# Kernel tuning notes

Measured on AMD Instinct MI355X. Metric: run time of the kernel, lower is better.

Reference implementation:

```python
import jax, jax.numpy as jnp
import numpy as np

C = 256
SHAPE = (4, 256, 32, 32, 32)  # B, C, D, H, W


def setup_inputs() -> dict:
    key = jax.random.key(0)
    ks = jax.random.split(key, 8)
    scale = 1.0 / np.sqrt(C)
    return {
        "x": jax.random.normal(ks[0], SHAPE, dtype=jnp.float32),
        "y": jax.random.normal(ks[1], SHAPE, dtype=jnp.float32),
        "Wq": jax.random.normal(ks[2], (C, C), dtype=jnp.float32) * scale,
        "bq": jax.random.normal(ks[3], (C,), dtype=jnp.float32) * 0.01,
        "Wk": jax.random.normal(ks[4], (C, C), dtype=jnp.float32) * scale,
        "bk": jax.random.normal(ks[5], (C,), dtype=jnp.float32) * 0.01,
        "Wv": jax.random.normal(ks[6], (C, C), dtype=jnp.float32) * scale,
        "bv": jax.random.normal(ks[7], (C,), dtype=jnp.float32) * 0.01,
    }


def _proj_flat(v, W, b):
    # 1x1x1 Conv3d == per-voxel linear over channels. v: [B,C,D,H,W] -> [B,C,N]
    B, Cc = v.shape[0], v.shape[1]
    vf = v.reshape(B, Cc, -1)  # [B, C, N]
    return jnp.einsum("oc,bcn->bon", W, vf) + b[None, :, None]


def reference(x, y, Wq, bq, Wk, bk, Wv, bv):
    spatial = y.shape[2:]
    q = _proj_flat(x, Wq, bq)  # [B, C, N]
    k = _proj_flat(y, Wk, bk)  # [B, C, N]
    v = _proj_flat(y, Wv, bv)  # [B, C, N]
    # channel-attention: scores[b, i, j] = sum_n q[b,i,n] * k[b,j,n]  (unscaled)
    scores = jnp.einsum("bin,bjn->bij", q, k)  # [B, C, C]
    weights = jax.nn.softmax(scores, axis=2)
    fused = jnp.einsum("bij,bjn->bin", weights, v)  # [B, C, N]
    return fused.reshape(fused.shape[0], fused.shape[1], *spatial)
```

## Files before the change

kernel.cpp:

```cpp
#include <hip/hip_runtime.h>

#define Bb 4
#define Cc 256
#define Nn 32768

typedef short s16x8 __attribute__((ext_vector_type(8)));
typedef float f32x4 __attribute__((ext_vector_type(4)));
typedef float f32x4v __attribute__((ext_vector_type(4)));

__device__ __forceinline__ unsigned short bfh(float f) {
    union { float f; unsigned u; } c; c.f = f;
    unsigned u = c.u + 0x7fffu + ((c.u >> 16) & 1u);
    return (unsigned short)(u >> 16);
}
__device__ __forceinline__ unsigned fbits(float f) {
    union { float f; unsigned u; } c; c.f = f; return c.u;
}
__device__ __forceinline__ float fof(unsigned u) {
    union { unsigned u; float f; } c; c.u = u; return c.f;
}
__device__ __forceinline__ int swz(int l) { return l ^ ((l >> 3) & 6); }

__device__ __forceinline__ void cvt8(f32x4v A, f32x4v B, uint4& h, uint4& l) {
    unsigned a0 = fbits(A.x), a1 = fbits(A.y), a2 = fbits(A.z), a3 = fbits(A.w);
    unsigned b0 = fbits(B.x), b1 = fbits(B.y), b2 = fbits(B.z), b3 = fbits(B.w);
    h.x = __builtin_amdgcn_perm(a1, a0, 0x07060302u);
    h.y = __builtin_amdgcn_perm(a3, a2, 0x07060302u);
    h.z = __builtin_amdgcn_perm(b1, b0, 0x07060302u);
    h.w = __builtin_amdgcn_perm(b3, b2, 0x07060302u);
    unsigned l0 = fbits(A.x - fof(a0 & 0xffff0000u)) + 0x8000u;
    unsigned l1 = fbits(A.y - fof(a1 & 0xffff0000u)) + 0x8000u;
    unsigned l2 = fbits(A.z - fof(a2 & 0xffff0000u)) + 0x8000u;
    unsigned l3 = fbits(A.w - fof(a3 & 0xffff0000u)) + 0x8000u;
    unsigned m0 = fbits(B.x - fof(b0 & 0xffff0000u)) + 0x8000u;
    unsigned m1 = fbits(B.y - fof(b1 & 0xffff0000u)) + 0x8000u;
    unsigned m2 = fbits(B.z - fof(b2 & 0xffff0000u)) + 0x8000u;
    unsigned m3 = fbits(B.w - fof(b3 & 0xffff0000u)) + 0x8000u;
    l.x = __builtin_amdgcn_perm(l1, l0, 0x07060302u);
    l.y = __builtin_amdgcn_perm(l3, l2, 0x07060302u);
    l.z = __builtin_amdgcn_perm(m1, m0, 0x07060302u);
    l.w = __builtin_amdgcn_perm(m3, m2, 0x07060302u);
}
__device__ __forceinline__ float s4(f32x4v v) { return (v.x + v.y) + (v.z + v.w); }

__global__ __launch_bounds__(512, 2) void k_gram(const float* __restrict__ x,
                                                 const float* __restrict__ y,
                                                 float* __restrict__ part,
                                                 float* __restrict__ sxp,
                                                 float* __restrict__ syp,
                                                 int nsplit) {
    extern __shared__ short smem[];

    int G = Bb * nsplit * 2;
    int chunk = G >> 3;
    int lid = blockIdx.x;
    int bid = (lid & 7) * chunk + (lid >> 3);

    int half = bid & 1;
    int ks = (bid >> 1) % nsplit;
    int b = bid / (2 * nsplit);
    int Kblk = Nn / nsplit;
    int nstep = Kblk >> 5;

    const float* X = x + (size_t)b * Cc * Nn + (size_t)(half * 128) * Nn + (size_t)ks * Kblk;
    const float* Y = y + (size_t)b * Cc * Nn + (size_t)ks * Kblk;

    int tid = threadIdx.x;
    int lane = tid & 63;
    int wave = tid >> 6;
    int wr = wave >> 2, wc = wave & 3;

    int xr = tid >> 2, xq = tid & 3;
    const float* px = X + (size_t)xr * Nn + xq * 8;
    int xl = (xr & 15) + 16 * xq;
    int xo = ((xr >> 4) * 64 + swz(xl)) * 8;
    int yr = tid >> 1, yh2 = tid & 1;
    const float* py = Y + (size_t)yr * Nn + yh2 * 16;
    int yl0 = (yr & 15) + 32 * yh2, yl1 = yl0 + 16;
    int yo0 = ((yr >> 4) * 64 + swz(yl0)) * 8;
    int yo1 = ((yr >> 4) * 64 + swz(yl1)) * 8;

    f32x4 acc[4][4];
    #pragma unroll
    for (int i = 0; i < 4; ++i)
        #pragma unroll
        for (int j = 0; j < 4; ++j)
            #pragma unroll
            for (int z = 0; z < 4; ++z) acc[i][j][z] = 0.f;

    float xsum = 0.f, ysum = 0.f;
    f32x4v A0[2], B0[4], A1[2], B1[4];

    #define LDX(A, B, kb) do { \
        A[0] = __builtin_nontemporal_load((const f32x4v*)(px + (kb)) + 0); \
        A[1] = __builtin_nontemporal_load((const f32x4v*)(px + (kb)) + 1); \
        B[0] = ((const f32x4v*)(py + (kb)))[0]; B[1] = ((const f32x4v*)(py + (kb)))[1]; \
        B[2] = ((const f32x4v*)(py + (kb)))[2]; B[3] = ((const f32x4v*)(py + (kb)))[3]; \
    } while (0)

    #define COMPUTE(Sb) do { \
        int sl = swz(lane); \
        s16x8 ah[4], al[4]; \
        _Pragma("unroll") \
        for (int i = 0; i < 4; ++i) { \
            int fr = (wr * 4 + i) * 64 + sl; \
            ah[i] = *(const s16x8*)&(Sb)[fr * 8]; \
            al[i] = *(const s16x8*)&(Sb)[4096 + fr * 8]; \
        } \
        _Pragma("unroll") \
        for (int j = 0; j < 4; ++j) { \
            int fr = (wc * 4 + j) * 64 + sl; \
            s16x8 bh = *(const s16x8*)&(Sb)[8192 + fr * 8]; \
            s16x8 bl = *(const s16x8*)&(Sb)[16384 + fr * 8]; \
            _Pragma("unroll") \
            for (int i = 0; i < 4; ++i) { \
                acc[i][j] = __builtin_amdgcn_mfma_f32_16x16x32_bf16(ah[i], bh, acc[i][j], 0, 0, 0); \
                acc[i][j] = __builtin_amdgcn_mfma_f32_16x16x32_bf16(ah[i], bl, acc[i][j], 0, 0, 0); \
                acc[i][j] = __builtin_amdgcn_mfma_f32_16x16x32_bf16(al[i], bh, acc[i][j], 0, 0, 0); \
            } \
        } \
    } while (0)

    #define GSTEP(A, B, nkb, donext, cur) do { \
        uint4 hx, qxv, hy0, qy0, hy1, qy1; \
        cvt8(A[0], A[1], hx, qxv); \
        cvt8(B[0], B[1], hy0, qy0); \
        cvt8(B[2], B[3], hy1, qy1); \
        xsum += s4(A[0]) + s4(A[1]); \
        if (half == 0) ysum += s4(B[0]) + s4(B[1]) + s4(B[2]) + s4(B[3]); \
        short* Sb = smem + (cur); \
        *(uint4*)&Sb[xo] = hx;  *(uint4*)&Sb[4096 + xo] = qxv; \
        *(uint4*)&Sb[8192 + yo0] = hy0; *(uint4*)&Sb[16384 + yo0] = qy0; \
        *(uint4*)&Sb[8192 + yo1] = hy1; *(uint4*)&Sb[16384 + yo1] = qy1; \
        if (donext) LDX(A, B, nkb); \
        asm volatile("s_waitcnt lgkmcnt(0)" ::: "memory"); \
        __builtin_amdgcn_sched_barrier(0); \
        __builtin_amdgcn_s_barrier(); \
        __builtin_amdgcn_sched_barrier(0); \
        COMPUTE(Sb); \
    } while (0)

    LDX(A0, B0, 0);
    LDX(A1, B1, 32);
    for (int t = 0; t < nstep; t += 2) {
        GSTEP(A0, B0, (t + 2) * 32, t + 2 < nstep, 0);
        GSTEP(A1, B1, (t + 3) * 32, t + 3 < nstep, 24576);
    }
    #undef GSTEP
    #undef COMPUTE
    #undef LDX

    xsum += __shfl_xor(xsum, 1);
    xsum += __shfl_xor(xsum, 2);
    ysum += __shfl_xor(ysum, 1);
    if (xq == 0) sxp[((size_t)b * nsplit + ks) * 256 + half * 128 + xr] = xsum;
    if (half == 0 && yh2 == 0) syp[((size_t)b * nsplit + ks) * 256 + yr] = ysum;

    float* P = part + ((size_t)b * nsplit + ks) * Cc * Cc;
    #pragma unroll
    for (int i = 0; i < 4; ++i)
        #pragma unroll
        for (int j = 0; j < 4; ++j)
            #pragma unroll
            for (int reg = 0; reg < 4; ++reg) {
                int gi = half * 128 + wr * 64 + i * 16 + (lane >> 4) * 4 + reg;
                int gj = wc * 64 + j * 16 + (lane & 15);
                P[(size_t)gi * Cc + gj] = acc[i][j][reg];
            }
}

__global__ __launch_bounds__(256) void k_reduceS(const float* __restrict__ part,
                                                 const float* __restrict__ sxp,
                                                 const float* __restrict__ syp,
                                                 float* __restrict__ S,
                                                 float* __restrict__ sx,
                                                 float* __restrict__ sy, int split) {
    if (blockIdx.x < 256) {
        int t = blockIdx.x * 256 + threadIdx.x;
        int b = t >> 14;
        int rc = t & 16383;
        f32x4v s = {0.f, 0.f, 0.f, 0.f};
        for (int ks = 0; ks < split; ++ks) {
            f32x4v v = ((const f32x4v*)(part + (((size_t)b * split + ks) << 16)))[rc];
            s += v;
        }
        ((f32x4v*)S)[t] = s;
    } else {
        int flat = (blockIdx.x - 256) * 256 + threadIdx.x;
        int b = flat >> 9, rem = flat & 511, which = rem >> 8, c = rem & 255;
        const float* src = (which ? syp : sxp) + (size_t)b * split * 256 + c;
        float s = 0.f;
        for (int ks = 0; ks < split; ++ks) s += src[(size_t)ks * 256];
        (which ? sy : sx)[b * 256 + c] = s;
    }
}

__global__ __launch_bounds__(256) void k_attn(const float* __restrict__ S,
                                              const float* __restrict__ sx,
                                              const float* __restrict__ sy,
                                              const float* __restrict__ Wq,
                                              const float* __restrict__ Wk,
                                              const float* __restrict__ Wv,
                                              const float* __restrict__ bq,
                                              const float* __restrict__ bk,
                                              const float* __restrict__ bv,
                                              short* __restrict__ Mbf,
                                              float* __restrict__ cb) {
    __shared__ float wq_lds[8][256];
    __shared__ float u_lds[8][256];
    __shared__ float p_lds[8][256];
    __shared__ float wv_lds[32][256];
    __shared__ float sx_lds[256], sy_lds[256];
    __shared__ float qx_lds[8];

    int b = blockIdx.x >> 5;
    int i0 = (blockIdx.x & 31) << 3;
    int tid = threadIdx.x;
    int lane = tid & 63, wv4 = tid >> 6;

    float bqv[8];
    #pragma unroll
    for (int ii = 0; ii < 8; ++ii) {
        wq_lds[ii][tid] = Wq[(size_t)(i0 + ii) * Cc + tid];
        bqv[ii] = bq[i0 + ii];
    }
    sx_lds[tid] = sx[b * Cc + tid];
    sy_lds[tid] = sy[b * Cc + tid];
    __syncthreads();

    float u[8] = {};
    const float* Sb = S + (size_t)b * Cc * Cc + tid;
    #pragma unroll 4
    for (int c = 0; c < Cc; ++c) {
        float s = Sb[(size_t)c * Cc];
        #pragma unroll
        for (int ii = 0; ii < 8; ++ii) u[ii] += wq_lds[ii][c] * s;
    }
    #pragma unroll
    for (int ii = 0; ii < 8; ++ii) u_lds[ii][tid] = u[ii] + bqv[ii] * sy_lds[tid];

    #pragma unroll
    for (int rr = 0; rr < 2; ++rr) {
        int ii = wv4 * 2 + rr;
        float p = 0.f;
        #pragma unroll
        for (int k = 0; k < 4; ++k) { int c = lane + 64 * k; p += wq_lds[ii][c] * sx_lds[c]; }
        #pragma unroll
        for (int m = 1; m < 64; m <<= 1) p += __shfl_xor(p, m);
        if (lane == 0) qx_lds[ii] = p;
    }
    __syncthreads();

    float sc[8] = {};
    const float* WkRow = Wk + (size_t)tid * Cc;
    for (int ch = 0; ch < 8; ++ch) {
        float wkr[32];
        #pragma unroll
        for (int k = 0; k < 8; ++k)
            *(float4*)&wkr[4 * k] = ((const float4*)(WkRow + ch * 32))[k];
        #pragma unroll
        for (int dd = 0; dd < 32; ++dd) {
            float w = wkr[dd];
            #pragma unroll
            for (int ii = 0; ii < 8; ++ii) sc[ii] += u_lds[ii][ch * 32 + dd] * w;
        }
    }
    float bkj = bk[tid];
    #pragma unroll
    for (int ii = 0; ii < 8; ++ii) {
        sc[ii] += (qx_lds[ii] + 32768.0f * bqv[ii]) * bkj;
        p_lds[ii][tid] = sc[ii];
    }
    __syncthreads();

    #pragma unroll
    for (int rr = 0; rr < 2; ++rr) {
        int ii = wv4 * 2 + rr;
        float v0 = p_lds[ii][lane], v1 = p_lds[ii][lane + 64];
        float v2 = p_lds[ii][lane + 128], v3 = p_lds[ii][lane + 192];
        float mx = fmaxf(fmaxf(v0, v1), fmaxf(v2, v3));
        #pragma unroll
        for (int m = 1; m < 64; m <<= 1) mx = fmaxf(mx, __shfl_xor(mx, m));
        float e0 = expf(v0 - mx), e1 = expf(v1 - mx), e2 = expf(v2 - mx), e3 = expf(v3 - mx);
        float ssum = (e0 + e1) + (e2 + e3);
        #pragma unroll
        for (int m = 1; m < 64; m <<= 1) ssum += __shfl_xor(ssum, m);
        float inv = 1.0f / ssum;
        float w0 = e0 * inv, w1 = e1 * inv, w2 = e2 * inv, w3 = e3 * inv;
        p_lds[ii][lane] = w0; p_lds[ii][lane + 64] = w1;
        p_lds[ii][lane + 128] = w2; p_lds[ii][lane + 192] = w3;
        float cbp = w0 * bv[lane] + w1 * bv[lane + 64] + w2 * bv[lane + 128] + w3 * bv[lane + 192];
        #pragma unroll
        for (int m = 1; m < 64; m <<= 1) cbp += __shfl_xor(cbp, m);
        if (lane == 0) cb[b * Cc + i0 + ii] = cbp;
    }
    __syncthreads();

    float m[8] = {};
    for (int jc = 0; jc < 8; ++jc) {
        #pragma unroll
        for (int k = 0; k < 8; ++k) {
            int fidx = k * 256 + tid;
            int jj = fidx >> 6, f4 = fidx & 63;
            *(float4*)&wv_lds[jj][4 * f4] =
                *(const float4*)(Wv + (size_t)(jc * 32 + jj) * Cc + 4 * f4);
        }
        __syncthreads();
        #pragma unroll 4
        for (int jj = 0; jj < 32; ++jj) {
            float w = wv_lds[jj][tid];
            #pragma unroll
            for (int ii = 0; ii < 8; ++ii) m[ii] += p_lds[ii][jc * 32 + jj] * w;
        }
        __syncthreads();
    }
    #pragma unroll
    for (int ii = 0; ii < 8; ++ii)
        Mbf[((size_t)(b * Cc + i0 + ii)) * Cc + tid] = (short)bfh(m[ii]);
}

__global__ __launch_bounds__(512, 2) void k_out_mfma(const short* __restrict__ Mbf,
                                                     const float* __restrict__ y,
                                                     const float* __restrict__ cb,
                                                     float* __restrict__ out) {
    int tid = threadIdx.x;
    int lane = tid & 63;
    int wave = tid >> 6;
    int wr = wave >> 2, wc = wave & 3;
    int bid = blockIdx.x;
    int b = bid >> 8, grp = bid & 255;
    int nbase = grp * 128 + wc * 32;
    const float* Y = y + (size_t)b * Cc * Nn;
    const short* M = Mbf + (size_t)b * Cc * Cc;
    int l15 = lane & 15;
    int cbase = 8 * (lane >> 4);
    int n0 = nbase + l15;

    f32x4 acc[8][2];
    #pragma unroll
    for (int ti = 0; ti < 8; ++ti)
        #pragma unroll
        for (int nb = 0; nb < 2; ++nb)
            #pragma unroll
            for (int z = 0; z < 4; ++z) acc[ti][nb][z] = 0.f;

    s16x8 af0[8], af1[8];
    float ya0[8], yb0[8], ya1[8], yb1[8];

    #define AFLD(AF, s) do { int c0 = 32 * (s) + cbase; \
        _Pragma("unroll") \
        for (int ti = 0; ti < 8; ++ti) \
            AF[ti] = *(const s16x8*)&M[(size_t)(wr * 128 + ti * 16 + l15) * Cc + c0]; \
        } while (0)

    #define LDY(YA, YB, s) do { int c0 = 32 * (s) + cbase; \
        _Pragma("unroll") \
        for (int j = 0; j < 8; ++j) { \
            YA[j] = Y[(size_t)(c0 + j) * Nn + n0]; \
            YB[j] = Y[(size_t)(c0 + j) * Nn + n0 + 16]; \
        } } while (0)

    #define OSTEP(AF, AFN, YA, YB, s) do { \
        s16x8 bf0, bf1; \
        _Pragma("unroll") \
        for (int j = 0; j < 8; ++j) { bf0[j] = (short)bfh(YA[j]); bf1[j] = (short)bfh(YB[j]); } \
        if ((s) + 1 < 8) AFLD(AFN, (s) + 1); \
        if ((s) + 2 < 8) LDY(YA, YB, (s) + 2); \
        _Pragma("unroll") \
        for (int ti = 0; ti < 8; ++ti) { \
            acc[ti][0] = __builtin_amdgcn_mfma_f32_16x16x32_bf16(AF[ti], bf0, acc[ti][0], 0, 0, 0); \
            acc[ti][1] = __builtin_amdgcn_mfma_f32_16x16x32_bf16(AF[ti], bf1, acc[ti][1], 0, 0, 0); \
        } } while (0)

    AFLD(af0, 0);
    LDY(ya0, yb0, 0);
    LDY(ya1, yb1, 1);
    for (int s = 0; s < 8; s += 2) {
        OSTEP(af0, af1, ya0, yb0, s);
        OSTEP(af1, af0, ya1, yb1, s + 1);
    }
    #undef OSTEP
    #undef LDY
    #undef AFLD

    #pragma unroll
    for (int ti = 0; ti < 8; ++ti)
        #pragma unroll
        for (int nb = 0; nb < 2; ++nb)
            #pragma unroll
            for (int reg = 0; reg < 4; ++reg) {
                int i = wr * 128 + ti * 16 + (lane >> 4) * 4 + reg;
                out[((size_t)b * Cc + i) * Nn + nbase + nb * 16 + l15] =
                    acc[ti][nb][reg] + cb[b * Cc + i];
            }
}

extern "C" void kernel_launch(void* const* d_in, const int* in_sizes, int n_in,
                              void* d_out, int out_size, void* d_ws, size_t ws_size,
                              hipStream_t stream) {
    const float* x  = (const float*)d_in[0];
    const float* y  = (const float*)d_in[1];
    const float* Wq = (const float*)d_in[2];
    const float* bq = (const float*)d_in[3];
    const float* Wk = (const float*)d_in[4];
    const float* bk = (const float*)d_in[5];
    const float* Wv = (const float*)d_in[6];
    const float* bv = (const float*)d_in[7];
    float* out = (float*)d_out;

    float* ws = (float*)d_ws;
    size_t off = 0;
    float* S  = ws + off; off += (size_t)Bb * Cc * Cc;
    float* sx = ws + off; off += Bb * Cc;
    float* sy = ws + off; off += Bb * Cc;
    short* Mbf = (short*)(ws + off); off += (size_t)Bb * Cc * Cc / 2;
    float* cb = ws + off; off += Bb * Cc;
    float* sxp = ws + off; off += (size_t)Bb * 64 * 256;
    float* syp = ws + off; off += (size_t)Bb * 64 * 256;
    float* part = ws + off;

    size_t avail = ws_size / 4 - off;
    int split = 32;
    while (split > 16 && (size_t)split * Bb * Cc * Cc > avail) split >>= 1;

    (void)hipFuncSetAttribute(reinterpret_cast<const void*>(k_gram),
                              hipFuncAttributeMaxDynamicSharedMemorySize, 98304);

    k_gram<<<Bb * split * 2, 512, 98304, stream>>>(x, y, part, sxp, syp, split);
    k_reduceS<<<264, 256, 0, stream>>>(part, sxp, syp, S, sx, sy, split);
    k_attn<<<Bb * 32, 256, 0, stream>>>(S, sx, sy, Wq, Wk, Wv, bq, bk, bv, Mbf, cb);
    k_out_mfma<<<1024, 512, 0, stream>>>(Mbf, y, cb, out);
}
```

Baseline: 221.1 us.

## Load gram MFMA operands directly from global into registers, dropping LDS staging

The gram kernel no longer stages bf16 hi/lo splits in shared memory behind a barrier. Each lane now loads its MFMA fragments straight from global memory, converts them in registers, and computes a 128x128 quadrant per 256-thread block, with four quadrant blocks per split. This removes LDS traffic and block barriers. In exchange the x and y data are each read twice from global memory across the quadrant blocks, and every lane reads 8 strided rows, which may hurt coalescing and raise register pressure.

```diff
diff --git a/kernel.cpp b/kernel.cpp
--- a/kernel.cpp
+++ b/kernel.cpp
@@ -19,7 +19,6 @@
 __device__ __forceinline__ float fof(unsigned u) {
     union { unsigned u; float f; } c; c.u = u; return c.f;
 }
-__device__ __forceinline__ int swz(int l) { return l ^ ((l >> 3) & 6); }
 
 __device__ __forceinline__ void cvt8(f32x4v A, f32x4v B, uint4& h, uint4& l) {
     unsigned a0 = fbits(A.x), a1 = fbits(A.y), a2 = fbits(A.z), a3 = fbits(A.w);
@@ -43,42 +42,39 @@
 }
 __device__ __forceinline__ float s4(f32x4v v) { return (v.x + v.y) + (v.z + v.w); }
 
-__global__ __launch_bounds__(512, 2) void k_gram(const float* __restrict__ x,
+__global__ __launch_bounds__(256, 2) void k_gram(const float* __restrict__ x,
                                                  const float* __restrict__ y,
                                                  float* __restrict__ part,
                                                  float* __restrict__ sxp,
                                                  float* __restrict__ syp,
                                                  int nsplit) {
-    extern __shared__ short smem[];
-
-    int G = Bb * nsplit * 2;
+    int G = Bb * nsplit * 4;
     int chunk = G >> 3;
     int lid = blockIdx.x;
     int bid = (lid & 7) * chunk + (lid >> 3);
 
-    int half = bid & 1;
-    int ks = (bid >> 1) % nsplit;
-    int b = bid / (2 * nsplit);
+    int quad = bid & 3;
+    int ti = quad >> 1, tj = quad & 1;
+    int ks = (bid >> 2) % nsplit;
+    int b  = bid / (4 * nsplit);
     int Kblk = Nn / nsplit;
     int nstep = Kblk >> 5;
-
-    const float* X = x + (size_t)b * Cc * Nn + (size_t)(half * 128) * Nn + (size_t)ks * Kblk;
-    const float* Y = y + (size_t)b * Cc * Nn + (size_t)ks * Kblk;
 
     int tid = threadIdx.x;
     int lane = tid & 63;
     int wave = tid >> 6;
-    int wr = wave >> 2, wc = wave & 3;
-
-    int xr = tid >> 2, xq = tid & 3;
-    const float* px = X + (size_t)xr * Nn + xq * 8;
-    int xl = (xr & 15) + 16 * xq;
-    int xo = ((xr >> 4) * 64 + swz(xl)) * 8;
-    int yr = tid >> 1, yh2 = tid & 1;
-    const float* py = Y + (size_t)yr * Nn + yh2 * 16;
-    int yl0 = (yr & 15) + 32 * yh2, yl1 = yl0 + 16;
-    int yo0 = ((yr >> 4) * 64 + swz(yl0)) * 8;
-    int yo1 = ((yr >> 4) * 64 + swz(yl1)) * 8;
+    int wwr = wave >> 1, wwc = wave & 1;
+    int l15 = lane & 15, lh = lane >> 4;
+
+    const float* Xb = x + (size_t)b * Cc * Nn + (size_t)ks * Kblk + lh * 8;
+    const float* Yb = y + (size_t)b * Cc * Nn + (size_t)ks * Kblk + lh * 8;
+    const float* ap[4];
+    const float* bp[4];
+    #pragma unroll
+    for (int i = 0; i < 4; ++i) {
+        ap[i] = Xb + (size_t)(ti * 128 + wwr * 64 + i * 16 + l15) * Nn;
+        bp[i] = Yb + (size_t)(tj * 128 + wwc * 64 + i * 16 + l15) * Nn;
+    }
 
     f32x4 acc[4][4];
     #pragma unroll
@@ -88,73 +84,72 @@
             #pragma unroll
             for (int z = 0; z < 4; ++z) acc[i][j][z] = 0.f;
 
-    float xsum = 0.f, ysum = 0.f;
-    f32x4v A0[2], B0[4], A1[2], B1[4];
-
-    #define LDX(A, B, kb) do { \
-        A[0] = __builtin_nontemporal_load((const f32x4v*)(px + (kb)) + 0); \
-        A[1] = __builtin_nontemporal_load((const f32x4v*)(px + (kb)) + 1); \
-        B[0] = ((const f32x4v*)(py + (kb)))[0]; B[1] = ((const f32x4v*)(py + (kb)))[1]; \
-        B[2] = ((const f32x4v*)(py + (kb)))[2]; B[3] = ((const f32x4v*)(py + (kb)))[3]; \
-    } while (0)
-
-    #define COMPUTE(Sb) do { \
-        int sl = swz(lane); \
-        s16x8 ah[4], al[4]; \
+    float xs[4] = {0.f, 0.f, 0.f, 0.f};
+    float ys[4] = {0.f, 0.f, 0.f, 0.f};
+
+    f32x4v A0[8], B0[8], A1[8], B1[8];
+
+    #define GLD(AS, BS, kb) do { \
         _Pragma("unroll") \
         for (int i = 0; i < 4; ++i) { \
-            int fr = (wr * 4 + i) * 64 + sl; \
-            ah[i] = *(const s16x8*)&(Sb)[fr * 8]; \
-            al[i] = *(const s16x8*)&(Sb)[4096 + fr * 8]; \
+            AS[2 * i]     = ((const f32x4v*)(ap[i] + (kb)))[0]; \
+            AS[2 * i + 1] = ((const f32x4v*)(ap[i] + (kb)))[1]; \
+            BS[2 * i]     = ((const f32x4v*)(bp[i] + (kb)))[0]; \
+            BS[2 * i + 1] = ((const f32x4v*)(bp[i] + (kb)))[1]; \
+        } } while (0)
+
+    #define GSTEP(AS, BS, nkb, donext) do { \
+        s16x8 Ah[4], Al[4], Bh[4], Bl[4]; \
+        _Pragma("unroll") \
+        for (int i = 0; i < 4; ++i) { \
+            uint4 h, q; \
+            cvt8(AS[2 * i], AS[2 * i + 1], h, q); \
+            Ah[i] = __builtin_bit_cast(s16x8, h); \
+            Al[i] = __builtin_bit_cast(s16x8, q); \
+            if (wwc == 0) xs[i] += s4(AS[2 * i]) + s4(AS[2 * i + 1]); \
+            cvt8(BS[2 * i], BS[2 * i + 1], h, q); \
+            Bh[i] = __builtin_bit_cast(s16x8, h); \
+            Bl[i] = __builtin_bit_cast(s16x8, q); \
+            if (wwr == 0) ys[i] += s4(BS[2 * i]) + s4(BS[2 * i + 1]); \
         } \
-        _Pragma("unroll") \
-        for (int j = 0; j < 4; ++j) { \
-            int fr = (wc * 4 + j) * 64 + sl; \
-            s16x8 bh = *(const s16x8*)&(Sb)[8192 + fr * 8]; \
-            s16x8 bl = *(const s16x8*)&(Sb)[16384 + fr * 8]; \
+        if (donext) GLD(AS, BS, nkb); \
+        _Pragma("unroll") \
+        for (int j = 0; j < 4; ++j) \
             _Pragma("unroll") \
             for (int i = 0; i < 4; ++i) { \
-                acc[i][j] = __builtin_amdgcn_mfma_f32_16x16x32_bf16(ah[i], bh, acc[i][j], 0, 0, 0); \
-                acc[i][j] = __builtin_amdgcn_mfma_f32_16x16x32_bf16(ah[i], bl, acc[i][j], 0, 0, 0); \
-                acc[i][j] = __builtin_amdgcn_mfma_f32_16x16x32_bf16(al[i], bh, acc[i][j], 0, 0, 0); \
+                acc[i][j] = __builtin_amdgcn_mfma_f32_16x16x32_bf16(Ah[i], Bh[j], acc[i][j], 0, 0, 0); \
+                acc[i][j] = __builtin_amdgcn_mfma_f32_16x16x32_bf16(Ah[i], Bl[j], acc[i][j], 0, 0, 0); \
+                acc[i][j] = __builtin_amdgcn_mfma_f32_16x16x32_bf16(Al[i], Bh[j], acc[i][j], 0, 0, 0); \
             } \
-        } \
-    } while (0)
-
-    #define GSTEP(A, B, nkb, donext, cur) do { \
-        uint4 hx, qxv, hy0, qy0, hy1, qy1; \
-        cvt8(A[0], A[1], hx, qxv); \
-        cvt8(B[0], B[1], hy0, qy0); \
-        cvt8(B[2], B[3], hy1, qy1); \
-        xsum += s4(A[0]) + s4(A[1]); \
-        if (half == 0) ysum += s4(B[0]) + s4(B[1]) + s4(B[2]) + s4(B[3]); \
-        short* Sb = smem + (cur); \
-        *(uint4*)&Sb[xo] = hx;  *(uint4*)&Sb[4096 + xo] = qxv; \
-        *(uint4*)&Sb[8192 + yo0] = hy0; *(uint4*)&Sb[16384 + yo0] = qy0; \
-        *(uint4*)&Sb[8192 + yo1] = hy1; *(uint4*)&Sb[16384 + yo1] = qy1; \
-        if (donext) LDX(A, B, nkb); \
-        asm volatile("s_waitcnt lgkmcnt(0)" ::: "memory"); \
-        __builtin_amdgcn_sched_barrier(0); \
-        __builtin_amdgcn_s_barrier(); \
-        __builtin_amdgcn_sched_barrier(0); \
-        COMPUTE(Sb); \
-    } while (0)
-
-    LDX(A0, B0, 0);
-    LDX(A1, B1, 32);
+        } while (0)
+
+    GLD(A0, B0, 0);
+    GLD(A1, B1, 32);
     for (int t = 0; t < nstep; t += 2) {
-        GSTEP(A0, B0, (t + 2) * 32, t + 2 < nstep, 0);
-        GSTEP(A1, B1, (t + 3) * 32, t + 3 < nstep, 24576);
+        GSTEP(A0, B0, (t + 2) * 32, t + 2 < nstep);
+        GSTEP(A1, B1, (t + 3) * 32, t + 3 < nstep);
     }
     #undef GSTEP
-    #undef COMPUTE
-    #undef LDX
-
-    xsum += __shfl_xor(xsum, 1);
-    xsum += __shfl_xor(xsum, 2);
-    ysum += __shfl_xor(ysum, 1);
-    if (xq == 0) sxp[((size_t)b * nsplit + ks) * 256 + half * 128 + xr] = xsum;
-    if (half == 0 && yh2 == 0) syp[((size_t)b * nsplit + ks) * 256 + yr] = ysum;
+    #undef GLD
+
+    #pragma unroll
+    for (int i = 0; i < 4; ++i) {
+        xs[i] += __shfl_xor(xs[i], 16);
+        xs[i] += __shfl_xor(xs[i], 32);
+        ys[i] += __shfl_xor(ys[i], 16);
+        ys[i] += __shfl_xor(ys[i], 32);
+    }
+    size_t sbase = ((size_t)b * nsplit + ks) * 256;
+    if (tj == 0 && wwc == 0 && lh == 0) {
+        #pragma unroll
+        for (int i = 0; i < 4; ++i)
+            sxp[sbase + ti * 128 + wwr * 64 + i * 16 + l15] = xs[i];
+    }
+    if (ti == 0 && wwr == 0 && lh == 0) {
+        #pragma unroll
+        for (int i = 0; i < 4; ++i)
+            syp[sbase + tj * 128 + wwc * 64 + i * 16 + l15] = ys[i];
+    }
 
     float* P = part + ((size_t)b * nsplit + ks) * Cc * Cc;
     #pragma unroll
@@ -163,8 +158,8 @@
         for (int j = 0; j < 4; ++j)
             #pragma unroll
             for (int reg = 0; reg < 4; ++reg) {
-                int gi = half * 128 + wr * 64 + i * 16 + (lane >> 4) * 4 + reg;
-                int gj = wc * 64 + j * 16 + (lane & 15);
+                int gi = ti * 128 + wwr * 64 + i * 16 + (lane >> 4) * 4 + reg;
+                int gj = tj * 128 + wwc * 64 + j * 16 + (lane & 15);
                 P[(size_t)gi * Cc + gj] = acc[i][j][reg];
             }
 }
@@ -423,10 +418,7 @@
     int split = 32;
     while (split > 16 && (size_t)split * Bb * Cc * Cc > avail) split >>= 1;
 
-    (void)hipFuncSetAttribute(reinterpret_cast<const void*>(k_gram),
-                              hipFuncAttributeMaxDynamicSharedMemorySize, 98304);
-
-    k_gram<<<Bb * split * 2, 512, 98304, stream>>>(x, y, part, sxp, syp, split);
+    k_gram<<<Bb * split * 4, 256, 0, stream>>>(x, y, part, sxp, syp, split);
     k_reduceS<<<264, 256, 0, stream>>>(part, sxp, syp, S, sx, sy, split);
     k_attn<<<Bb * 32, 256, 0, stream>>>(S, sx, sy, Wq, Wk, Wv, bq, bk, bv, Mbf, cb);
     k_out_mfma<<<1024, 512, 0, stream>>>(Mbf, y, cb, out);
```

Result: slower. 552.1 us (+149.7%).
